# Kernel optimization log

Measured on AMD Instinct MI355X. Metric: run time of the kernel, lower is better.

## Reference

```python
import jax, jax.numpy as jnp
import numpy as np

D_MODEL = 512
D_QK = 512
H = 8
HEAD_DIM = D_QK // H   # 64
V_DIM = D_MODEL // H   # 64
PROJ_OUT = D_MODEL + 2 * D_QK + H  # 1544


def setup_inputs() -> dict:
    key = jax.random.key(0)
    k1, k2, k3, k4, k5 = jax.random.split(key, 5)
    B, S = 2, 2048
    x = jax.random.normal(k1, (B, S, D_MODEL), dtype=jnp.float32)
    s_in = 1.0 / np.sqrt(D_MODEL)
    Wvqkn_w = jax.random.uniform(k2, (PROJ_OUT, D_MODEL), jnp.float32, -s_in, s_in)
    Wvqkn_b = jax.random.uniform(k3, (PROJ_OUT,), jnp.float32, -s_in, s_in)
    out_w = jax.random.uniform(k4, (D_MODEL, D_MODEL), jnp.float32, -s_in, s_in)
    out_b = jax.random.uniform(k5, (D_MODEL,), jnp.float32, -s_in, s_in)
    return {"x": x, "Wvqkn_w": Wvqkn_w, "Wvqkn_b": Wvqkn_b,
            "out_w": out_w, "out_b": out_b}


def reference(x, Wvqkn_w, Wvqkn_b, out_w, out_b):
    B, S, _ = x.shape
    # fused qkvn projection
    vqkn = jnp.einsum('bsd,od->bso', x, Wvqkn_w) + Wvqkn_b  # [B,S,1544]
    v = vqkn[..., :D_MODEL]                                  # [B,S,512]
    qk = vqkn[..., D_MODEL:D_MODEL + 2 * D_QK]               # [B,S,1024]
    n = vqkn[..., D_MODEL + 2 * D_QK:]                       # [B,S,H]
    qk = qk.reshape(B, S, 2, H, HEAD_DIM)
    v = v.reshape(B, S, H, V_DIM)
    q, k = qk[:, :, 0], qk[:, :, 1]                          # approx_fn = identity
    # linear attention via cumulative KV state (scale=1.0, scale_B=False)
    kv = jnp.einsum('bshd,bsht->bshdt', k, v)                # [B,S,H,D,Dv]
    kv = jnp.cumsum(kv, axis=1)
    out = jnp.einsum('bshd,bshdt->bsht', q, kv)              # [B,S,H,Dv]
    # normalization gating: norm_fn = exp, no offset
    gate = jnp.exp(-jnp.exp(n))                              # [B,S,H]
    ctx = gate[..., None] * out
    ctx = ctx.reshape(B, S, D_MODEL)
    return jnp.einsum('bsd,od->bso', ctx, out_w) + out_b
```

## Files before the change

kernel.cpp:

```cpp
#include <hip/hip_runtime.h>
#include <hip/hip_bf16.h>
#include <math.h>

#define B_    2
#define S_    2048
#define DM    512
#define H_    8
#define PROJ  1544
#define NPAD1 1664
#define CHK   64
#define NC    32
#define BS_   4096
#define BH    16

typedef __attribute__((ext_vector_type(8))) short shortx8;
typedef __attribute__((ext_vector_type(4))) short shortx4;
typedef __attribute__((ext_vector_type(4))) float floatx4;

#define GCAST(p) ((const __attribute__((address_space(1))) void*)(p))
#define LCAST(p) ((__attribute__((address_space(3))) void*)(p))

__device__ inline short f2bf(float f) {
    __hip_bfloat16 h = __float2bfloat16(f);
    return *(short*)&h;
}
__device__ inline float bf2f(short s) {
    __hip_bfloat16 h = *(__hip_bfloat16*)&s;
    return __bfloat162float(h);
}
__device__ inline shortx8 read8(const short* buf, int row, int k) {
    return *(const shortx8*)&buf[row * 64 + ((((k >> 3) ^ (row & 7))) << 3)];
}

__global__ __launch_bounds__(256) void convert_pad(const float* __restrict__ src,
                                                   short* __restrict__ dst,
                                                   int srcRows, int dstRows, int K) {
    int t = blockIdx.x * 256 + threadIdx.x;
    long e0 = (long)t * 8;
    if (e0 >= (long)dstRows * K) return;
    int row = (int)(e0 / K);
    short out[8];
    if (row < srcRows) {
        const float* s = src + e0;
        float4 f0 = *(const float4*)s;
        float4 f1 = *(const float4*)(s + 4);
        out[0] = f2bf(f0.x); out[1] = f2bf(f0.y); out[2] = f2bf(f0.z); out[3] = f2bf(f0.w);
        out[4] = f2bf(f1.x); out[5] = f2bf(f1.y); out[6] = f2bf(f1.z); out[7] = f2bf(f1.w);
    } else {
#pragma unroll
        for (int i = 0; i < 8; i++) out[i] = 0;
    }
    *(shortx8*)(dst + e0) = *(shortx8*)out;
}

__global__ __launch_bounds__(256) void gemm_mfma(const short* __restrict__ A,
                                                 const short* __restrict__ Bw,
                                                 const float* __restrict__ bias,
                                                 float* __restrict__ C,
                                                 int Nstore, int K) {
    __shared__ short As[128 * 32];
    __shared__ short Bs[128 * 32];
    const int tid  = threadIdx.x;
    const int wave = tid >> 6, lane = tid & 63;
    const int m0 = blockIdx.y * 128;
    const int n0 = blockIdx.x * 128;
    const int srow  = tid >> 2;
    const int skoff = (tid & 3) * 8;
    const int lm = lane & 15, q = lane >> 4;
    const int wr = (wave >> 1) * 64, wc = (wave & 1) * 64;
    floatx4 acc[4][4] = {};

    const short* gA0 = A  + (size_t)(m0 + srow) * K + skoff;
    const short* gA1 = A  + (size_t)(m0 + 64 + srow) * K + skoff;
    const short* gB0 = Bw + (size_t)(n0 + srow) * K + skoff;
    const short* gB1 = Bw + (size_t)(n0 + 64 + srow) * K + skoff;

    for (int k0 = 0; k0 < K; k0 += 32) {
        __builtin_amdgcn_global_load_lds(GCAST(gA0 + k0), LCAST(&As[wave * 512]),        16, 0, 0);
        __builtin_amdgcn_global_load_lds(GCAST(gA1 + k0), LCAST(&As[2048 + wave * 512]), 16, 0, 0);
        __builtin_amdgcn_global_load_lds(GCAST(gB0 + k0), LCAST(&Bs[wave * 512]),        16, 0, 0);
        __builtin_amdgcn_global_load_lds(GCAST(gB1 + k0), LCAST(&Bs[2048 + wave * 512]), 16, 0, 0);
        __syncthreads();

        shortx8 af[4], bw[4];
#pragma unroll
        for (int i = 0; i < 4; i++)
            af[i] = *(const shortx8*)&As[(wr + i * 16 + lm) * 32 + q * 8];
#pragma unroll
        for (int j = 0; j < 4; j++)
            bw[j] = *(const shortx8*)&Bs[(wc + j * 16 + lm) * 32 + q * 8];
#pragma unroll
        for (int i = 0; i < 4; i++)
#pragma unroll
            for (int j = 0; j < 4; j++)
                acc[i][j] = __builtin_amdgcn_mfma_f32_16x16x32_bf16(af[i], bw[j], acc[i][j], 0, 0, 0);
        __syncthreads();
    }
#pragma unroll
    for (int i = 0; i < 4; i++) {
        int rb = m0 + wr + i * 16 + q * 4;
#pragma unroll
        for (int j = 0; j < 4; j++) {
            int col = n0 + wc + j * 16 + lm;
            if (col < Nstore) {
                float bv = bias[col];
#pragma unroll
                for (int r = 0; r < 4; r++)
                    C[(size_t)(rb + r) * Nstore + col] = acc[i][j][r] + bv;
            }
        }
    }
}

__global__ __launch_bounds__(256) void gemm1_fused(const short* __restrict__ A,
                                                   const short* __restrict__ Bw,
                                                   const float* __restrict__ bias,
                                                   short* __restrict__ qb,
                                                   short* __restrict__ kb,
                                                   short* __restrict__ kTb,
                                                   short* __restrict__ vTb,
                                                   float* __restrict__ gateb) {
    __shared__ short As[128 * 32];
    __shared__ short Bs[128 * 32];
    const int K = DM;
    const int tid  = threadIdx.x;
    const int wave = tid >> 6, lane = tid & 63;
    const int m0 = blockIdx.y * 128;
    const int n0 = blockIdx.x * 128;
    const int srow  = tid >> 2;
    const int skoff = (tid & 3) * 8;
    const int lm = lane & 15, q = lane >> 4;
    const int wr = (wave >> 1) * 64, wc = (wave & 1) * 64;
    floatx4 acc[4][4] = {};

    const short* gA0 = A  + (size_t)(m0 + srow) * K + skoff;
    const short* gA1 = A  + (size_t)(m0 + 64 + srow) * K + skoff;
    const short* gB0 = Bw + (size_t)(n0 + srow) * K + skoff;
    const short* gB1 = Bw + (size_t)(n0 + 64 + srow) * K + skoff;

    for (int k0 = 0; k0 < K; k0 += 32) {
        __builtin_amdgcn_global_load_lds(GCAST(gA0 + k0), LCAST(&As[wave * 512]),        16, 0, 0);
        __builtin_amdgcn_global_load_lds(GCAST(gA1 + k0), LCAST(&As[2048 + wave * 512]), 16, 0, 0);
        __builtin_amdgcn_global_load_lds(GCAST(gB0 + k0), LCAST(&Bs[wave * 512]),        16, 0, 0);
        __builtin_amdgcn_global_load_lds(GCAST(gB1 + k0), LCAST(&Bs[2048 + wave * 512]), 16, 0, 0);
        __syncthreads();

        shortx8 af[4], bw[4];
#pragma unroll
        for (int i = 0; i < 4; i++)
            af[i] = *(const shortx8*)&As[(wr + i * 16 + lm) * 32 + q * 8];
#pragma unroll
        for (int j = 0; j < 4; j++)
            bw[j] = *(const shortx8*)&Bs[(wc + j * 16 + lm) * 32 + q * 8];
#pragma unroll
        for (int i = 0; i < 4; i++)
#pragma unroll
            for (int j = 0; j < 4; j++)
                acc[i][j] = __builtin_amdgcn_mfma_f32_16x16x32_bf16(af[i], bw[j], acc[i][j], 0, 0, 0);
        __syncthreads();
    }

    const int bIdx = m0 >> 11;
    const int bh0  = bIdx * H_;
#pragma unroll
    for (int i = 0; i < 4; i++) {
        int s0 = (m0 & (S_ - 1)) + wr + i * 16 + q * 4;
#pragma unroll
        for (int j = 0; j < 4; j++) {
            int col = n0 + wc + j * 16 + lm;
            float bv = (col < PROJ) ? bias[col] : 0.f;
            float vals[4];
#pragma unroll
            for (int r = 0; r < 4; r++) vals[r] = acc[i][j][r] + bv;
            if (col < 512) {
                int h = col >> 6, vd = col & 63;
                short tmp[4];
#pragma unroll
                for (int r = 0; r < 4; r++) tmp[r] = f2bf(vals[r]);
                *(shortx4*)&vTb[((size_t)(bh0 + h) * 64 + vd) * S_ + s0] = *(shortx4*)tmp;
            } else if (col < 1024) {
                int h = (col >> 6) - 8, d = col & 63;
                size_t rb = ((size_t)(bh0 + h) * S_ + s0) * 64 + d;
#pragma unroll
                for (int r = 0; r < 4; r++) qb[rb + (size_t)r * 64] = f2bf(vals[r]);
            } else if (col < 1536) {
                int h = (col >> 6) - 16, d = col & 63;
                size_t rb = ((size_t)(bh0 + h) * S_ + s0) * 64 + d;
                short tmp[4];
#pragma unroll
                for (int r = 0; r < 4; r++) { tmp[r] = f2bf(vals[r]); kb[rb + (size_t)r * 64] = tmp[r]; }
                *(shortx4*)&kTb[((size_t)(bh0 + h) * 64 + d) * S_ + s0] = *(shortx4*)tmp;
            } else if (col < PROJ) {
                int h = col - 1536;
                float g[4];
#pragma unroll
                for (int r = 0; r < 4; r++) g[r] = __expf(-__expf(vals[r]));
                *(float4*)&gateb[(size_t)(bh0 + h) * S_ + s0] = make_float4(g[0], g[1], g[2], g[3]);
            }
        }
    }
}

__global__ __launch_bounds__(256) void chunk_kv_mfma(const short* __restrict__ vTb,
                                                     const short* __restrict__ kTb,
                                                     float* __restrict__ kvbuf) {
    __shared__ __align__(16) short VT[64 * 64];
    __shared__ __align__(16) short KT[64 * 64];
    const int blk = blockIdx.x;
    const int c = blk & (NC - 1), bh = blk >> 5;
    const int base = c * CHK;
    const int tid = threadIdx.x, wave = tid >> 6, lane = tid & 63;
    const int lrow = lane >> 3, lgrp = lane & 7;

#pragma unroll
    for (int half = 0; half < 2; half++) {
        int v0 = wave * 8 + half * 32;
        int row = v0 + lrow;
        int gcol = ((lgrp ^ (row & 7)) << 3);
        __builtin_amdgcn_global_load_lds(GCAST(vTb + ((size_t)(bh * 64 + row)) * S_ + base + gcol),
                                         LCAST(&VT[v0 * 64]), 16, 0, 0);
        __builtin_amdgcn_global_load_lds(GCAST(kTb + ((size_t)(bh * 64 + row)) * S_ + base + gcol),
                                         LCAST(&KT[v0 * 64]), 16, 0, 0);
    }
    __syncthreads();

    const int lm = lane & 15, q = lane >> 4;
    const int wr = (wave >> 1) * 32, wc = (wave & 1) * 32;
    floatx4 acc[2][2] = {};
#pragma unroll
    for (int ks = 0; ks < 2; ks++) {
        shortx8 a[2], b2[2];
#pragma unroll
        for (int i = 0; i < 2; i++) a[i]  = read8(VT, wr + i * 16 + lm, ks * 32 + q * 8);
#pragma unroll
        for (int j = 0; j < 2; j++) b2[j] = read8(KT, wc + j * 16 + lm, ks * 32 + q * 8);
#pragma unroll
        for (int i = 0; i < 2; i++)
#pragma unroll
            for (int j = 0; j < 2; j++)
                acc[i][j] = __builtin_amdgcn_mfma_f32_16x16x32_bf16(a[i], b2[j], acc[i][j], 0, 0, 0);
    }
    float* outp = kvbuf + ((size_t)blk << 12);
#pragma unroll
    for (int i = 0; i < 2; i++)
#pragma unroll
        for (int j = 0; j < 2; j++)
#pragma unroll
            for (int r = 0; r < 4; r++)
                outp[(wr + i * 16 + q * 4 + r) * 64 + wc + j * 16 + lm] = acc[i][j][r];
}

__global__ __launch_bounds__(256) void scan_kv(float* __restrict__ kvbuf) {
    const int blk = blockIdx.x;
    const int bh = blk >> 4, seg = blk & 15;
    const int e = seg * 256 + threadIdx.x;
    float* p = kvbuf + (((size_t)bh * NC) << 12) + e;
    float run = 0.f;
#pragma unroll 4
    for (int c = 0; c < NC; c++) {
        float cur = p[(size_t)c << 12];
        p[(size_t)c << 12] = run;
        run += cur;
    }
}

__global__ __launch_bounds__(256) void attn_mfma(const short* __restrict__ qb,
                                                 const short* __restrict__ kb,
                                                 const short* __restrict__ vTb,
                                                 const float* __restrict__ gateb,
                                                 const float* __restrict__ kvbuf,
                                                 short* __restrict__ ctxb) {
    __shared__ __align__(16) short Qs[64 * 64];
    __shared__ __align__(16) short Ks[64 * 64];
    __shared__ __align__(16) short VTs[64 * 64];
    __shared__ __align__(16) short Phi[64 * 64];
    __shared__ __align__(16) short Plo[64 * 64];
    __shared__ __align__(16) short Sb[64 * 72];
    __shared__ float gs[64];
    const int blk = blockIdx.x;
    const int c = blk & (NC - 1), bh = blk >> 5;
    const int base = c * CHK;
    const int tid = threadIdx.x, wave = tid >> 6, lane = tid & 63;
    const int lrow = lane >> 3, lgrp = lane & 7;

#pragma unroll
    for (int half = 0; half < 2; half++) {
        int v0 = wave * 8 + half * 32;
        int row = v0 + lrow;
        int gcol = ((lgrp ^ (row & 7)) << 3);
        __builtin_amdgcn_global_load_lds(GCAST(qb + ((size_t)bh * S_ + base + row) * 64 + gcol),
                                         LCAST(&Qs[v0 * 64]), 16, 0, 0);
        __builtin_amdgcn_global_load_lds(GCAST(kb + ((size_t)bh * S_ + base + row) * 64 + gcol),
                                         LCAST(&Ks[v0 * 64]), 16, 0, 0);
        __builtin_amdgcn_global_load_lds(GCAST(vTb + ((size_t)(bh * 64 + row)) * S_ + base + gcol),
                                         LCAST(&VTs[v0 * 64]), 16, 0, 0);
    }
    const float* kvp = kvbuf + ((size_t)blk << 12);
#pragma unroll
    for (int it = 0; it < 16; it++) {
        int idx = it * 256 + tid;
        int v = idx >> 6, d = idx & 63;
        float f = kvp[idx];
        short hi = f2bf(f);
        short lo = f2bf(f - bf2f(hi));
        int sw = v * 64 + (((d >> 3) ^ (v & 7)) << 3) + (d & 7);
        Phi[sw] = hi; Plo[sw] = lo;
    }
    if (tid < 64) gs[tid] = gateb[(size_t)bh * S_ + base + tid];
    __syncthreads();

    const int lm = lane & 15, q = lane >> 4;
    const int wr = (wave >> 1) * 32, wc = (wave & 1) * 32;

    floatx4 sacc[2][2] = {};
#pragma unroll
    for (int ks = 0; ks < 2; ks++) {
        shortx8 qa[2], kf[2];
#pragma unroll
        for (int i = 0; i < 2; i++) qa[i] = read8(Qs, wr + i * 16 + lm, ks * 32 + q * 8);
#pragma unroll
        for (int j = 0; j < 2; j++) kf[j] = read8(Ks, wc + j * 16 + lm, ks * 32 + q * 8);
#pragma unroll
        for (int i = 0; i < 2; i++)
#pragma unroll
            for (int j = 0; j < 2; j++)
                sacc[i][j] = __builtin_amdgcn_mfma_f32_16x16x32_bf16(qa[i], kf[j], sacc[i][j], 0, 0, 0);
    }
#pragma unroll
    for (int i = 0; i < 2; i++)
#pragma unroll
        for (int j = 0; j < 2; j++)
#pragma unroll
            for (int r = 0; r < 4; r++) {
                int s = wr + i * 16 + q * 4 + r;
                int t = wc + j * 16 + lm;
                Sb[s * 72 + t] = f2bf(t <= s ? sacc[i][j][r] : 0.f);
            }
    __syncthreads();

    floatx4 oacc[2][2] = {};
#pragma unroll
    for (int ks = 0; ks < 2; ks++) {
        shortx8 sa[2], vb[2];
#pragma unroll
        for (int i = 0; i < 2; i++)
            sa[i] = *(const shortx8*)&Sb[(wr + i * 16 + lm) * 72 + ks * 32 + q * 8];
#pragma unroll
        for (int j = 0; j < 2; j++) vb[j] = read8(VTs, wc + j * 16 + lm, ks * 32 + q * 8);
#pragma unroll
        for (int i = 0; i < 2; i++)
#pragma unroll
            for (int j = 0; j < 2; j++)
                oacc[i][j] = __builtin_amdgcn_mfma_f32_16x16x32_bf16(sa[i], vb[j], oacc[i][j], 0, 0, 0);
    }
#pragma unroll
    for (int ks = 0; ks < 2; ks++) {
        shortx8 qa[2], ph[2], pl[2];
#pragma unroll
        for (int i = 0; i < 2; i++) qa[i] = read8(Qs, wr + i * 16 + lm, ks * 32 + q * 8);
#pragma unroll
        for (int j = 0; j < 2; j++) {
            ph[j] = read8(Phi, wc + j * 16 + lm, ks * 32 + q * 8);
            pl[j] = read8(Plo, wc + j * 16 + lm, ks * 32 + q * 8);
        }
#pragma unroll
        for (int i = 0; i < 2; i++)
#pragma unroll
            for (int j = 0; j < 2; j++) {
                oacc[i][j] = __builtin_amdgcn_mfma_f32_16x16x32_bf16(qa[i], ph[j], oacc[i][j], 0, 0, 0);
                oacc[i][j] = __builtin_amdgcn_mfma_f32_16x16x32_bf16(qa[i], pl[j], oacc[i][j], 0, 0, 0);
            }
    }
    const size_t tok0 = (size_t)(bh >> 3) * S_ + base;
    const int h = bh & 7;
#pragma unroll
    for (int i = 0; i < 2; i++)
#pragma unroll
        for (int j = 0; j < 2; j++)
#pragma unroll
            for (int r = 0; r < 4; r++) {
                int s = wr + i * 16 + q * 4 + r;
                int v = wc + j * 16 + lm;
                ctxb[(tok0 + s) * DM + h * 64 + v] = f2bf(gs[s] * oacc[i][j][r]);
            }
}

extern "C" void kernel_launch(void* const* d_in, const int* in_sizes, int n_in,
                              void* d_out, int out_size, void* d_ws, size_t ws_size,
                              hipStream_t stream) {
    const float* x       = (const float*)d_in[0];
    const float* Wvqkn_w = (const float*)d_in[1];
    const float* Wvqkn_b = (const float*)d_in[2];
    const float* out_w   = (const float*)d_in[3];
    const float* out_b   = (const float*)d_in[4];
    float* out = (float*)d_out;

    float* kvbuf = (float*)d_ws;
    short* xb    = (short*)(kvbuf + (size_t)BH * NC * 4096);
    short* w1b   = xb   + (size_t)BS_ * DM;
    short* w2b   = w1b  + (size_t)NPAD1 * DM;
    short* ctxb  = w2b  + (size_t)DM * DM;
    short* qb    = ctxb + (size_t)BS_ * DM;
    short* kb    = qb   + (size_t)BH * S_ * 64;
    short* kTb   = kb   + (size_t)BH * S_ * 64;
    short* vTb   = kTb  + (size_t)BH * S_ * 64;
    float* gateb = (float*)(vTb + (size_t)BH * S_ * 64);

    convert_pad<<<(BS_ * DM / 8 + 255) / 256, 256, 0, stream>>>(x, xb, BS_, BS_, DM);
    convert_pad<<<(NPAD1 * DM / 8 + 255) / 256, 256, 0, stream>>>(Wvqkn_w, w1b, PROJ, NPAD1, DM);
    convert_pad<<<(DM * DM / 8 + 255) / 256, 256, 0, stream>>>(out_w, w2b, DM, DM, DM);

    gemm1_fused<<<dim3(NPAD1 / 128, BS_ / 128), 256, 0, stream>>>(
        xb, w1b, Wvqkn_b, qb, kb, kTb, vTb, gateb);

    chunk_kv_mfma<<<BH * NC, 256, 0, stream>>>(vTb, kTb, kvbuf);
    scan_kv<<<BH * 16, 256, 0, stream>>>(kvbuf);
    attn_mfma<<<BH * NC, 256, 0, stream>>>(qb, kb, vTb, gateb, kvbuf, ctxb);

    gemm_mfma<<<dim3(DM / 128, BS_ / 128), 256, 0, stream>>>(ctxb, w2b, out_b, out, DM, DM);
}
```

Measured before the change: 125.9 us.

## Merge conversions, drop scan kernel, shrink GEMM M-tiles to 64

Three conversion launches become one kernel, which removes launch overhead. The separate scan_kv kernel is removed. Each attention block now sums the prefix KV states of all earlier chunks itself, and blocks are ordered longest-first. Both GEMMs move from 128x128 to 64x128 tiles to double the block count and improve occupancy on the many CUs. The trade-off is redundant prefix reads in attention (up to 31 chunk states per block) and less data reuse per GEMM tile.

```diff
diff --git a/kernel.cpp b/kernel.cpp
--- a/kernel.cpp
+++ b/kernel.cpp
@@ -32,82 +32,92 @@
     return *(const shortx8*)&buf[row * 64 + ((((k >> 3) ^ (row & 7))) << 3)];
 }
 
-__global__ __launch_bounds__(256) void convert_pad(const float* __restrict__ src,
-                                                   short* __restrict__ dst,
-                                                   int srcRows, int dstRows, int K) {
-    int t = blockIdx.x * 256 + threadIdx.x;
-    long e0 = (long)t * 8;
-    if (e0 >= (long)dstRows * K) return;
-    int row = (int)(e0 / K);
+#define E1 ((size_t)BS_ * DM)
+#define E2 ((size_t)NPAD1 * DM)
+#define E3 ((size_t)DM * DM)
+__global__ __launch_bounds__(256) void convert_all(const float* __restrict__ x,
+                                                   const float* __restrict__ w1,
+                                                   const float* __restrict__ w2,
+                                                   short* __restrict__ xb,
+                                                   short* __restrict__ w1b,
+                                                   short* __restrict__ w2b) {
+    size_t e = ((size_t)blockIdx.x * 256 + threadIdx.x) * 8;
+    const float* src;
+    short* dst;
+    bool zero = false;
+    if (e < E1) { src = x + e; dst = xb + e; }
+    else if (e < E1 + E2) {
+        size_t o = e - E1;
+        dst = w1b + o;
+        size_t row = o >> 9;
+        if (row < PROJ) src = w1 + o; else { src = w1; zero = true; }
+    } else if (e < E1 + E2 + E3) {
+        size_t o = e - E1 - E2;
+        src = w2 + o; dst = w2b + o;
+    } else return;
     short out[8];
-    if (row < srcRows) {
-        const float* s = src + e0;
-        float4 f0 = *(const float4*)s;
-        float4 f1 = *(const float4*)(s + 4);
+    if (zero) {
+#pragma unroll
+        for (int i = 0; i < 8; i++) out[i] = 0;
+    } else {
+        float4 f0 = *(const float4*)src;
+        float4 f1 = *(const float4*)(src + 4);
         out[0] = f2bf(f0.x); out[1] = f2bf(f0.y); out[2] = f2bf(f0.z); out[3] = f2bf(f0.w);
         out[4] = f2bf(f1.x); out[5] = f2bf(f1.y); out[6] = f2bf(f1.z); out[7] = f2bf(f1.w);
-    } else {
-#pragma unroll
-        for (int i = 0; i < 8; i++) out[i] = 0;
-    }
-    *(shortx8*)(dst + e0) = *(shortx8*)out;
-}
-
-__global__ __launch_bounds__(256) void gemm_mfma(const short* __restrict__ A,
-                                                 const short* __restrict__ Bw,
-                                                 const float* __restrict__ bias,
-                                                 float* __restrict__ C,
-                                                 int Nstore, int K) {
-    __shared__ short As[128 * 32];
+    }
+    *(shortx8*)dst = *(shortx8*)out;
+}
+
+__global__ __launch_bounds__(256) void gemm_mfma64(const short* __restrict__ A,
+                                                   const short* __restrict__ Bw,
+                                                   const float* __restrict__ bias,
+                                                   float* __restrict__ C,
+                                                   int N, int K) {
+    __shared__ short As[64 * 32];
     __shared__ short Bs[128 * 32];
     const int tid  = threadIdx.x;
     const int wave = tid >> 6, lane = tid & 63;
-    const int m0 = blockIdx.y * 128;
+    const int m0 = blockIdx.y * 64;
     const int n0 = blockIdx.x * 128;
-    const int srow  = tid >> 2;
-    const int skoff = (tid & 3) * 8;
+    const int srow  = lane >> 2;
+    const int skoff = (lane & 3) * 8;
     const int lm = lane & 15, q = lane >> 4;
-    const int wr = (wave >> 1) * 64, wc = (wave & 1) * 64;
-    floatx4 acc[4][4] = {};
-
-    const short* gA0 = A  + (size_t)(m0 + srow) * K + skoff;
-    const short* gA1 = A  + (size_t)(m0 + 64 + srow) * K + skoff;
-    const short* gB0 = Bw + (size_t)(n0 + srow) * K + skoff;
-    const short* gB1 = Bw + (size_t)(n0 + 64 + srow) * K + skoff;
+    const int wc = wave * 32;
+    floatx4 acc[4][2] = {};
+
+    const short* gA  = A  + (size_t)(m0 + wave * 16 + srow) * K + skoff;
+    const short* gB0 = Bw + (size_t)(n0 + wave * 16 + srow) * K + skoff;
+    const short* gB1 = Bw + (size_t)(n0 + 64 + wave * 16 + srow) * K + skoff;
 
     for (int k0 = 0; k0 < K; k0 += 32) {
-        __builtin_amdgcn_global_load_lds(GCAST(gA0 + k0), LCAST(&As[wave * 512]),        16, 0, 0);
-        __builtin_amdgcn_global_load_lds(GCAST(gA1 + k0), LCAST(&As[2048 + wave * 512]), 16, 0, 0);
+        __builtin_amdgcn_global_load_lds(GCAST(gA  + k0), LCAST(&As[wave * 512]),        16, 0, 0);
         __builtin_amdgcn_global_load_lds(GCAST(gB0 + k0), LCAST(&Bs[wave * 512]),        16, 0, 0);
         __builtin_amdgcn_global_load_lds(GCAST(gB1 + k0), LCAST(&Bs[2048 + wave * 512]), 16, 0, 0);
         __syncthreads();
-
-        shortx8 af[4], bw[4];
+        shortx8 af[4], bw[2];
 #pragma unroll
         for (int i = 0; i < 4; i++)
-            af[i] = *(const shortx8*)&As[(wr + i * 16 + lm) * 32 + q * 8];
-#pragma unroll
-        for (int j = 0; j < 4; j++)
+            af[i] = *(const shortx8*)&As[(i * 16 + lm) * 32 + q * 8];
+#pragma unroll
+        for (int j = 0; j < 2; j++)
             bw[j] = *(const shortx8*)&Bs[(wc + j * 16 + lm) * 32 + q * 8];
 #pragma unroll
         for (int i = 0; i < 4; i++)
 #pragma unroll
-            for (int j = 0; j < 4; j++)
+            for (int j = 0; j < 2; j++)
                 acc[i][j] = __builtin_amdgcn_mfma_f32_16x16x32_bf16(af[i], bw[j], acc[i][j], 0, 0, 0);
         __syncthreads();
     }
 #pragma unroll
     for (int i = 0; i < 4; i++) {
-        int rb = m0 + wr + i * 16 + q * 4;
-#pragma unroll
-        for (int j = 0; j < 4; j++) {
+        int rb = m0 + i * 16 + q * 4;
+#pragma unroll
+        for (int j = 0; j < 2; j++) {
             int col = n0 + wc + j * 16 + lm;
-            if (col < Nstore) {
-                float bv = bias[col];
-#pragma unroll
-                for (int r = 0; r < 4; r++)
-                    C[(size_t)(rb + r) * Nstore + col] = acc[i][j][r] + bv;
-            }
+            float bv = bias[col];
+#pragma unroll
+            for (int r = 0; r < 4; r++)
+                C[(size_t)(rb + r) * N + col] = acc[i][j][r] + bv;
         }
     }
 }
@@ -120,42 +130,39 @@
                                                    short* __restrict__ kTb,
                                                    short* __restrict__ vTb,
                                                    float* __restrict__ gateb) {
-    __shared__ short As[128 * 32];
+    __shared__ short As[64 * 32];
     __shared__ short Bs[128 * 32];
     const int K = DM;
     const int tid  = threadIdx.x;
     const int wave = tid >> 6, lane = tid & 63;
-    const int m0 = blockIdx.y * 128;
+    const int m0 = blockIdx.y * 64;
     const int n0 = blockIdx.x * 128;
-    const int srow  = tid >> 2;
-    const int skoff = (tid & 3) * 8;
+    const int srow  = lane >> 2;
+    const int skoff = (lane & 3) * 8;
     const int lm = lane & 15, q = lane >> 4;
-    const int wr = (wave >> 1) * 64, wc = (wave & 1) * 64;
-    floatx4 acc[4][4] = {};
-
-    const short* gA0 = A  + (size_t)(m0 + srow) * K + skoff;
-    const short* gA1 = A  + (size_t)(m0 + 64 + srow) * K + skoff;
-    const short* gB0 = Bw + (size_t)(n0 + srow) * K + skoff;
-    const short* gB1 = Bw + (size_t)(n0 + 64 + srow) * K + skoff;
+    const int wc = wave * 32;
+    floatx4 acc[4][2] = {};
+
+    const short* gA  = A  + (size_t)(m0 + wave * 16 + srow) * K + skoff;
+    const short* gB0 = Bw + (size_t)(n0 + wave * 16 + srow) * K + skoff;
+    const short* gB1 = Bw + (size_t)(n0 + 64 + wave * 16 + srow) * K + skoff;
 
     for (int k0 = 0; k0 < K; k0 += 32) {
-        __builtin_amdgcn_global_load_lds(GCAST(gA0 + k0), LCAST(&As[wave * 512]),        16, 0, 0);
-        __builtin_amdgcn_global_load_lds(GCAST(gA1 + k0), LCAST(&As[2048 + wave * 512]), 16, 0, 0);
+        __builtin_amdgcn_global_load_lds(GCAST(gA  + k0), LCAST(&As[wave * 512]),        16, 0, 0);
         __builtin_amdgcn_global_load_lds(GCAST(gB0 + k0), LCAST(&Bs[wave * 512]),        16, 0, 0);
         __builtin_amdgcn_global_load_lds(GCAST(gB1 + k0), LCAST(&Bs[2048 + wave * 512]), 16, 0, 0);
         __syncthreads();
-
-        shortx8 af[4], bw[4];
+        shortx8 af[4], bw[2];
 #pragma unroll
         for (int i = 0; i < 4; i++)
-            af[i] = *(const shortx8*)&As[(wr + i * 16 + lm) * 32 + q * 8];
-#pragma unroll
-        for (int j = 0; j < 4; j++)
+            af[i] = *(const shortx8*)&As[(i * 16 + lm) * 32 + q * 8];
+#pragma unroll
+        for (int j = 0; j < 2; j++)
             bw[j] = *(const shortx8*)&Bs[(wc + j * 16 + lm) * 32 + q * 8];
 #pragma unroll
         for (int i = 0; i < 4; i++)
 #pragma unroll
-            for (int j = 0; j < 4; j++)
+            for (int j = 0; j < 2; j++)
                 acc[i][j] = __builtin_amdgcn_mfma_f32_16x16x32_bf16(af[i], bw[j], acc[i][j], 0, 0, 0);
         __syncthreads();
     }
@@ -164,9 +171,9 @@
     const int bh0  = bIdx * H_;
 #pragma unroll
     for (int i = 0; i < 4; i++) {
-        int s0 = (m0 & (S_ - 1)) + wr + i * 16 + q * 4;
-#pragma unroll
-        for (int j = 0; j < 4; j++) {
+        int s0 = (m0 & (S_ - 1)) + i * 16 + q * 4;
+#pragma unroll
+        for (int j = 0; j < 2; j++) {
             int col = n0 + wc + j * 16 + lm;
             float bv = (col < PROJ) ? bias[col] : 0.f;
             float vals[4];
@@ -248,20 +255,6 @@
 #pragma unroll
             for (int r = 0; r < 4; r++)
                 outp[(wr + i * 16 + q * 4 + r) * 64 + wc + j * 16 + lm] = acc[i][j][r];
-}
-
-__global__ __launch_bounds__(256) void scan_kv(float* __restrict__ kvbuf) {
-    const int blk = blockIdx.x;
-    const int bh = blk >> 4, seg = blk & 15;
-    const int e = seg * 256 + threadIdx.x;
-    float* p = kvbuf + (((size_t)bh * NC) << 12) + e;
-    float run = 0.f;
-#pragma unroll 4
-    for (int c = 0; c < NC; c++) {
-        float cur = p[(size_t)c << 12];
-        p[(size_t)c << 12] = run;
-        run += cur;
-    }
 }
 
 __global__ __launch_bounds__(256) void attn_mfma(const short* __restrict__ qb,
@@ -278,7 +271,8 @@
     __shared__ __align__(16) short Sb[64 * 72];
     __shared__ float gs[64];
     const int blk = blockIdx.x;
-    const int c = blk & (NC - 1), bh = blk >> 5;
+    const int bh = blk & (BH - 1);
+    const int c  = (NC - 1) - (blk >> 4);
     const int base = c * CHK;
     const int tid = threadIdx.x, wave = tid >> 6, lane = tid & 63;
     const int lrow = lane >> 3, lgrp = lane & 7;
@@ -295,12 +289,21 @@
         __builtin_amdgcn_global_load_lds(GCAST(vTb + ((size_t)(bh * 64 + row)) * S_ + base + gcol),
                                          LCAST(&VTs[v0 * 64]), 16, 0, 0);
     }
-    const float* kvp = kvbuf + ((size_t)blk << 12);
+
+    float pacc[16] = {};
+    {
+        const float* kvb = kvbuf + (((size_t)bh * NC) << 12) + tid;
+        for (int cp = 0; cp < c; cp++) {
+            const float* p = kvb + ((size_t)cp << 12);
+#pragma unroll
+            for (int it = 0; it < 16; it++) pacc[it] += p[it * 256];
+        }
+    }
 #pragma unroll
     for (int it = 0; it < 16; it++) {
         int idx = it * 256 + tid;
         int v = idx >> 6, d = idx & 63;
-        float f = kvp[idx];
+        float f = pacc[it];
         short hi = f2bf(f);
         short lo = f2bf(f - bf2f(hi));
         int sw = v * 64 + (((d >> 3) ^ (v & 7)) << 3) + (d & 7);
@@ -406,16 +409,14 @@
     short* vTb   = kTb  + (size_t)BH * S_ * 64;
     float* gateb = (float*)(vTb + (size_t)BH * S_ * 64);
 
-    convert_pad<<<(BS_ * DM / 8 + 255) / 256, 256, 0, stream>>>(x, xb, BS_, BS_, DM);
-    convert_pad<<<(NPAD1 * DM / 8 + 255) / 256, 256, 0, stream>>>(Wvqkn_w, w1b, PROJ, NPAD1, DM);
-    convert_pad<<<(DM * DM / 8 + 255) / 256, 256, 0, stream>>>(out_w, w2b, DM, DM, DM);
-
-    gemm1_fused<<<dim3(NPAD1 / 128, BS_ / 128), 256, 0, stream>>>(
+    convert_all<<<(int)((E1 + E2 + E3) / 8 / 256), 256, 0, stream>>>(
+        x, Wvqkn_w, out_w, xb, w1b, w2b);
+
+    gemm1_fused<<<dim3(NPAD1 / 128, BS_ / 64), 256, 0, stream>>>(
         xb, w1b, Wvqkn_b, qb, kb, kTb, vTb, gateb);
 
     chunk_kv_mfma<<<BH * NC, 256, 0, stream>>>(vTb, kTb, kvbuf);
-    scan_kv<<<BH * 16, 256, 0, stream>>>(kvbuf);
     attn_mfma<<<BH * NC, 256, 0, stream>>>(qb, kb, vTb, gateb, kvbuf, ctxb);
 
-    gemm_mfma<<<dim3(DM / 128, BS_ / 128), 256, 0, stream>>>(ctxb, w2b, out_b, out, DM, DM);
-}
+    gemm_mfma64<<<dim3(DM / 128, BS_ / 64), 256, 0, stream>>>(ctxb, w2b, out_b, out, DM, DM);
+}
```

Result: faster. 121.2 us (-3.8%).
